# Kernel tuning notes

Measured on AMD Instinct MI355X. Metric: run time of the kernel, lower is better.

## Reference

```python
import jax, jax.numpy as jnp
import numpy as np

B, S, D, H, A = 4, 2048, 512, 8, 64


def setup_inputs() -> dict:
    key = jax.random.key(0)
    ks = jax.random.split(key, 12)
    inv_d = 1.0 / np.sqrt(D)
    inv_ha = 1.0 / np.sqrt(H * A)
    return {
        "query": jax.random.normal(ks[0], (B, S, D), jnp.float32),
        "key": jax.random.normal(ks[1], (B, S, D), jnp.float32),
        "value": jax.random.normal(ks[2], (B, S, D), jnp.float32),
        # stacked per-head projection weights, layout [H, in, out] so y = x @ W + b
        "Wq": jax.random.uniform(ks[3], (H, D, A), jnp.float32, -inv_d, inv_d),
        "bq": jax.random.uniform(ks[4], (H, A), jnp.float32, -inv_d, inv_d),
        "Wk": jax.random.uniform(ks[5], (H, D, A), jnp.float32, -inv_d, inv_d),
        "bk": jax.random.uniform(ks[6], (H, A), jnp.float32, -inv_d, inv_d),
        "Wv": jax.random.uniform(ks[7], (H, D, A), jnp.float32, -inv_d, inv_d),
        "bv": jax.random.uniform(ks[8], (H, A), jnp.float32, -inv_d, inv_d),
        "Wo": jax.random.uniform(ks[9], (H * A, D), jnp.float32, -inv_ha, inv_ha),
        "bo": jax.random.uniform(ks[10], (D,), jnp.float32, -inv_ha, inv_ha),
    }


def reference(query, key, value, Wq, bq, Wk, bk, Wv, bv, Wo, bo):
    b, s, _ = query.shape
    h, _, a = Wq.shape
    # per-head projections, batched across heads: [B,H,S,A]
    q = jnp.einsum("bsd,hda->bhsa", query, Wq) + bq[None, :, None, :]
    k = jnp.einsum("bsd,hda->bhsa", key, Wk) + bk[None, :, None, :]
    v = jnp.einsum("bsd,hda->bhsa", value, Wv) + bv[None, :, None, :]
    scale = a ** 0.5
    scores = jnp.einsum("bhqa,bhka->bhqk", q, k) / scale  # [B,H,S,S]
    # Faithful to original: subsequent_mask has 0.0 on lower tri, -inf above;
    # masked_fill(mask == 0, -1e9) therefore masks the LOWER triangle (incl diag).
    tril = jnp.tril(jnp.ones((s, s), dtype=bool))
    scores = jnp.where(tril, jnp.float32(-1e9), scores)
    attn = jax.nn.softmax(scores, axis=-1)
    out = jnp.einsum("bhqk,bhka->bhqa", attn, v)  # [B,H,S,A]
    # concat heads in order (head-major in feature dim, matching torch.cat dim=-1)
    out = out.transpose(0, 2, 1, 3).reshape(b, s, h * a)
    return out @ Wo + bo
```

## Files before the change

kernel.cpp:

```cpp
#include <hip/hip_runtime.h>
#include <hip/hip_bf16.h>

#define B_ 4
#define S_ 2048
#define D_ 512
#define H_ 8
#define A_ 64

typedef __attribute__((ext_vector_type(8))) __bf16 bf16x8;
typedef __attribute__((ext_vector_type(4))) __bf16 bf16x4;
typedef __attribute__((ext_vector_type(4))) float f32x4;

static __device__ __forceinline__ f32x4 mfma16(bf16x8 a, bf16x8 b, f32x4 c) {
  return __builtin_amdgcn_mfma_f32_16x16x32_bf16(a, b, c, 0, 0, 0);
}

static __device__ __forceinline__ f32x4 zero4() {
  f32x4 z = {0.f, 0.f, 0.f, 0.f};
  return z;
}

#define QSCALE 0.18033688011f

#if __has_builtin(__builtin_amdgcn_exp2f)
#define EXP2(x) __builtin_amdgcn_exp2f(x)
#else
#define EXP2(x) exp2f(x)
#endif

#define GLDS(g, l)                                                      \
  __builtin_amdgcn_global_load_lds(                                     \
      (const __attribute__((address_space(1))) void*)(g),               \
      (__attribute__((address_space(3))) void*)(l), 16, 0, 0)

__global__ void prep_all_kernel(const float* __restrict__ q, const float* __restrict__ k,
                                const float* __restrict__ v,
                                const float* __restrict__ Wq, const float* __restrict__ Wk,
                                const float* __restrict__ Wv, const float* __restrict__ Wo,
                                __bf16* __restrict__ xq, __bf16* __restrict__ xk,
                                __bf16* __restrict__ xv,
                                __bf16* __restrict__ tq, __bf16* __restrict__ tk,
                                __bf16* __restrict__ tv, __bf16* __restrict__ to_) {
  __shared__ float tile[64][65];
  if (blockIdx.x < 12288) {
    int idx = blockIdx.x * 256 + threadIdx.x;
    int which = idx >> 20;
    int i = idx & ((1 << 20) - 1);
    const float4* s = (const float4*)(which == 0 ? q : (which == 1 ? k : v));
    __bf16* d = (which == 0) ? xq : (which == 1 ? xk : xv);
    float4 f = s[i];
    bf16x4 o;
    o.x = (__bf16)f.x; o.y = (__bf16)f.y; o.z = (__bf16)f.z; o.w = (__bf16)f.w;
    *(bf16x4*)(d + 4 * i) = o;
  } else {
    int t = blockIdx.x - 12288;
    if (t < 192) {
      int mat = t >> 6;
      int h = (t >> 3) & 7;
      int d0 = (t & 7) * 64;
      const float* W = (mat == 0) ? Wq : (mat == 1 ? Wk : Wv);
      __bf16* dst = (mat == 0) ? tq : (mat == 1 ? tk : tv);
      float sc = (mat == 0) ? QSCALE : 1.0f;
      int a = threadIdx.x & 63, r0 = threadIdx.x >> 6;
#pragma unroll
      for (int i = 0; i < 16; i++) {
        int dd = r0 * 16 + i;
        tile[dd][a] = W[(h * D_ + d0 + dd) * A_ + a] * sc;
      }
      __syncthreads();
      int dd = threadIdx.x & 63, a0 = threadIdx.x >> 6;
#pragma unroll
      for (int i = 0; i < 16; i++) {
        int a2 = a0 * 16 + i;
        dst[(h * 64 + a2) * D_ + d0 + dd] = (__bf16)tile[dd][a2];
      }
    } else {
      int t2 = t - 192;
      int f0 = (t2 >> 3) * 64, d0 = (t2 & 7) * 64;
      int d = threadIdx.x & 63, r0 = threadIdx.x >> 6;
#pragma unroll
      for (int i = 0; i < 16; i++) {
        int ff = r0 * 16 + i;
        tile[ff][d] = Wo[(f0 + ff) * D_ + d0 + d];
      }
      __syncthreads();
      int f = threadIdx.x & 63, a0 = threadIdx.x >> 6;
#pragma unroll
      for (int i = 0; i < 16; i++) {
        int dd = a0 * 16 + i;
        to_[(d0 + dd) * D_ + f0 + f] = (__bf16)tile[f][dd];
      }
    }
  }
}

__global__ __launch_bounds__(256) void proj_gemm_kernel(
    const __bf16* __restrict__ Xq, const __bf16* __restrict__ Xk, const __bf16* __restrict__ Xv,
    const __bf16* __restrict__ Wtq, const __bf16* __restrict__ Wtk, const __bf16* __restrict__ Wtv,
    const float* __restrict__ bq, const float* __restrict__ bk, const float* __restrict__ bv,
    __bf16* __restrict__ Qb, __bf16* __restrict__ Kb, __bf16* __restrict__ Vtb) {
  int z = blockIdx.z;
  const __bf16* X  = (z == 0) ? Xq  : (z == 1 ? Xk  : Xv);
  const __bf16* Wt = (z == 0) ? Wtq : (z == 1 ? Wtk : Wtv);
  const float* bias = (z == 0) ? bq : (z == 1 ? bk : bv);
  float bscale = (z == 0) ? QSCALE : 1.0f;

  int lane = threadIdx.x & 63, wv = threadIdx.x >> 6;
  int wr = wv >> 1, wc = wv & 1;
  int quad = lane >> 4, lc = lane & 15;
  int M0 = blockIdx.x * 128, N0 = blockIdx.y * 128;
  int m0 = M0 + wr * 64, n0 = N0 + wc * 64;

  __shared__ __align__(16) __bf16 smem[2 * 2 * 128 * 64];
#define AB(buf) (smem + (buf) * 16384)
#define BB(buf) (smem + (buf) * 16384 + 8192)

  int srow = lane >> 3;
  int sg = ((lane & 7) ^ srow) * 8;

#pragma unroll
  for (int i = 0; i < 4; ++i) {
    int r0 = wv * 32 + i * 8;
    GLDS(X  + (M0 + r0 + srow) * D_ + sg, AB(0) + r0 * 64);
    GLDS(Wt + (N0 + r0 + srow) * D_ + sg, BB(0) + r0 * 64);
  }

  f32x4 acc[4][4];
#pragma unroll
  for (int mt = 0; mt < 4; mt++)
#pragma unroll
    for (int nt = 0; nt < 4; nt++) acc[mt][nt] = zero4();

  __syncthreads();

  for (int j = 0; j < 8; ++j) {
    int cb = j & 1;
    if (j < 7) {
      int k0 = (j + 1) * 64;
#pragma unroll
      for (int i = 0; i < 4; ++i) {
        int r0 = wv * 32 + i * 8;
        GLDS(X  + (M0 + r0 + srow) * D_ + k0 + sg, AB(cb ^ 1) + r0 * 64);
        GLDS(Wt + (N0 + r0 + srow) * D_ + k0 + sg, BB(cb ^ 1) + r0 * 64);
      }
    }
    const __bf16* Al = AB(cb);
    const __bf16* Bl = BB(cb);
#pragma unroll
    for (int kk = 0; kk < 2; ++kk) {
      int gp = ((kk * 4 + quad) ^ (lc & 7)) * 8;
      bf16x8 a[4], bb[4];
#pragma unroll
      for (int mt = 0; mt < 4; mt++)
        a[mt] = *(const bf16x8*)(Al + (wr * 64 + mt * 16 + lc) * 64 + gp);
#pragma unroll
      for (int nt = 0; nt < 4; nt++)
        bb[nt] = *(const bf16x8*)(Bl + (wc * 64 + nt * 16 + lc) * 64 + gp);
#pragma unroll
      for (int mt = 0; mt < 4; mt++)
#pragma unroll
        for (int nt = 0; nt < 4; nt++)
          acc[mt][nt] = mfma16(a[mt], bb[nt], acc[mt][nt]);
    }
    __syncthreads();
  }

  __bf16* vlds = smem + wv * (64 * 72);

  int h = n0 >> 6;
  int b = m0 >> 11, s0 = m0 & (S_ - 1);
  if (z < 2) {
#pragma unroll
    for (int nt = 0; nt < 4; nt++) {
      int col = n0 + nt * 16 + lc;
      float bval = bias[col] * bscale;
#pragma unroll
      for (int mt = 0; mt < 4; mt++)
#pragma unroll
        for (int r = 0; r < 4; r++)
          vlds[(mt * 16 + quad * 4 + r) * 72 + nt * 16 + lc] = (__bf16)(acc[mt][nt][r] + bval);
    }
    __asm__ volatile("s_waitcnt lgkmcnt(0)" ::: "memory");
    __bf16* dst = (z == 0) ? Qb : Kb;
#pragma unroll
    for (int it = 0; it < 8; it++) {
      int row = it * 8 + (lane >> 3);
      int c8 = (lane & 7) * 8;
      bf16x8 vv = *(const bf16x8*)(vlds + row * 72 + c8);
      *(bf16x8*)(dst + ((b * H_ + h) * S_ + s0 + row) * A_ + c8) = vv;
    }
  } else {
#pragma unroll
    for (int nt = 0; nt < 4; nt++) {
      int col = n0 + nt * 16 + lc;
      float bval = bias[col];
#pragma unroll
      for (int mt = 0; mt < 4; mt++) {
        bf16x4 pk;
#pragma unroll
        for (int r = 0; r < 4; r++) pk[r] = (__bf16)(acc[mt][nt][r] + bval);
        *(bf16x4*)(vlds + (nt * 16 + lc) * 72 + mt * 16 + quad * 4) = pk;
      }
    }
    __asm__ volatile("s_waitcnt lgkmcnt(0)" ::: "memory");
#pragma unroll
    for (int it = 0; it < 8; it++) {
      int a_l = it * 8 + (lane >> 3);
      int s_l = (lane & 7) * 8;
      bf16x8 vvv = *(const bf16x8*)(vlds + a_l * 72 + s_l);
      *(bf16x8*)(Vtb + ((b * H_ + h) * A_ + a_l) * S_ + s0 + s_l) = vvv;
    }
  }
}

__global__ __launch_bounds__(256, 4) void flash_kernel(const __bf16* __restrict__ Q,
                                                       const __bf16* __restrict__ K,
                                                       const __bf16* __restrict__ Vt,
                                                       __bf16* __restrict__ O) {
  int id = blockIdx.x;
  int xcd = id & 7, slot = id >> 3;
  int bh = xcd * 4 + (slot & 3);
  int beta = slot >> 2;
  int lane = threadIdx.x & 63, wv = threadIdx.x >> 6;
  int quad = lane >> 4, lc = lane & 15;
  int R0 = beta * 128 + wv * 32;
  int ntile = 32 - 2 * beta;
  int t0 = 2 * beta;

  const __bf16* Qp = Q + bh * S_ * A_;
  const __bf16* Kp = K + bh * S_ * A_;
  const __bf16* Vp = Vt + bh * A_ * S_;

  __shared__ __align__(16) __bf16 kvbuf[2][2][64][64];
  __shared__ __align__(16) __bf16 plds_all[4][32][72];
  __bf16* plds = &plds_all[wv][0][0];

  int srow = lane >> 3;
  int sg = ((lane & 7) ^ srow) * 8;

  {
    int kt = t0 << 6;
#pragma unroll
    for (int i = 0; i < 2; ++i) {
      int r0 = wv * 16 + i * 8;
      GLDS(Kp + (kt + r0 + srow) * A_ + sg, &kvbuf[0][0][r0][0]);
      GLDS(Vp + (r0 + srow) * S_ + kt + sg, &kvbuf[0][1][r0][0]);
    }
  }

  bf16x8 qf[2][2];
#pragma unroll
  for (int qt = 0; qt < 2; qt++) {
    qf[qt][0] = *(const bf16x8*)(Qp + (R0 + qt * 16 + lc) * A_ + quad * 8);
    qf[qt][1] = *(const bf16x8*)(Qp + (R0 + qt * 16 + lc) * A_ + 32 + quad * 8);
  }

  f32x4 o[2][4];
  float lsum[2][4];
#pragma unroll
  for (int qt = 0; qt < 2; qt++)
#pragma unroll
    for (int t = 0; t < 4; t++) { o[qt][t] = zero4(); lsum[qt][t] = 0.f; }

  int g0 = (quad ^ (lc & 7)) * 8;
  int g1 = ((quad + 4) ^ (lc & 7)) * 8;

  __syncthreads();

  for (int j = 0; j < ntile; ++j) {
    int t = t0 + j;
    int cb = j & 1;
    if (j + 1 < ntile) {
      int ktn = (t + 1) << 6;
#pragma unroll
      for (int i = 0; i < 2; ++i) {
        int r0 = wv * 16 + i * 8;
        GLDS(Kp + (ktn + r0 + srow) * A_ + sg, &kvbuf[cb ^ 1][0][r0][0]);
        GLDS(Vp + (r0 + srow) * S_ + ktn + sg, &kvbuf[cb ^ 1][1][r0][0]);
      }
    }
    bool skip = (t * 64 + 63 <= R0);
    if (!skip) {
      const __bf16* Kl = &kvbuf[cb][0][0][0];
      const __bf16* Vl = &kvbuf[cb][1][0][0];
      f32x4 sc[2][4];
#pragma unroll
      for (int nt = 0; nt < 4; nt++) {
        int rr = nt * 16 + lc;
        bf16x8 kf0 = *(const bf16x8*)(Kl + rr * 64 + g0);
        bf16x8 kf1 = *(const bf16x8*)(Kl + rr * 64 + g1);
#pragma unroll
        for (int qt = 0; qt < 2; qt++) {
          f32x4 ss = zero4();
          ss = mfma16(qf[qt][0], kf0, ss);
          ss = mfma16(qf[qt][1], kf1, ss);
          sc[qt][nt] = ss;
        }
      }
      if (t * 64 < R0 + 32) {
#pragma unroll
        for (int qt = 0; qt < 2; qt++)
#pragma unroll
          for (int nt = 0; nt < 4; nt++) {
            int col = t * 64 + nt * 16 + lc;
#pragma unroll
            for (int r = 0; r < 4; r++) {
              int row = R0 + qt * 16 + quad * 4 + r;
              float pv = (col <= row) ? 0.0f : EXP2(sc[qt][nt][r]);
              lsum[qt][r] += pv;
              plds[(qt * 16 + quad * 4 + r) * 72 + nt * 16 + lc] = (__bf16)pv;
            }
          }
      } else {
#pragma unroll
        for (int qt = 0; qt < 2; qt++)
#pragma unroll
          for (int nt = 0; nt < 4; nt++)
#pragma unroll
            for (int r = 0; r < 4; r++) {
              float pv = EXP2(sc[qt][nt][r]);
              lsum[qt][r] += pv;
              plds[(qt * 16 + quad * 4 + r) * 72 + nt * 16 + lc] = (__bf16)pv;
            }
      }
      __asm__ volatile("s_waitcnt lgkmcnt(0)" ::: "memory");
      bf16x8 pf[2][2];
#pragma unroll
      for (int qt = 0; qt < 2; qt++) {
        pf[qt][0] = *(const bf16x8*)(plds + (qt * 16 + lc) * 72 + quad * 8);
        pf[qt][1] = *(const bf16x8*)(plds + (qt * 16 + lc) * 72 + 32 + quad * 8);
      }
      __builtin_amdgcn_s_setprio(1);
#pragma unroll
      for (int ot = 0; ot < 4; ot++) {
        int rr = ot * 16 + lc;
        bf16x8 vf0 = *(const bf16x8*)(Vl + rr * 64 + g0);
        bf16x8 vf1 = *(const bf16x8*)(Vl + rr * 64 + g1);
#pragma unroll
        for (int qt = 0; qt < 2; qt++) {
          o[qt][ot] = mfma16(pf[qt][0], vf0, o[qt][ot]);
          o[qt][ot] = mfma16(pf[qt][1], vf1, o[qt][ot]);
        }
      }
      __builtin_amdgcn_s_setprio(0);
    }
    __syncthreads();
  }

#pragma unroll
  for (int qt = 0; qt < 2; qt++)
#pragma unroll
    for (int r = 0; r < 4; r++) {
      float l = lsum[qt][r];
#pragma unroll
      for (int off = 1; off < 16; off <<= 1) l += __shfl_xor(l, off, 64);
      lsum[qt][r] = l;
    }

#pragma unroll
  for (int qt = 0; qt < 2; qt++)
#pragma unroll
    for (int r = 0; r < 4; r++) {
      float rl = 1.0f / lsum[qt][r];
#pragma unroll
      for (int ot = 0; ot < 4; ot++)
        plds[(qt * 16 + quad * 4 + r) * 72 + ot * 16 + lc] = (__bf16)(o[qt][ot][r] * rl);
    }
  __asm__ volatile("s_waitcnt lgkmcnt(0)" ::: "memory");
  int b = bh >> 3, h = bh & 7;
#pragma unroll
  for (int it = 0; it < 4; it++) {
    int row = it * 8 + (lane >> 3);
    int c8 = (lane & 7) * 8;
    int grow = R0 + row;
    if (grow != S_ - 1)
      *(bf16x8*)(O + (b * S_ + grow) * (H_ * A_) + h * 64 + c8) =
          *(const bf16x8*)(plds + row * 72 + c8);
  }
}

__global__ void rowfix_kernel(const __bf16* __restrict__ Vt, __bf16* __restrict__ O) {
  int bh = blockIdx.x;
  int a = blockIdx.y * 8 + (threadIdx.x >> 5);
  int li = threadIdx.x & 31;
  const __bf16* src = Vt + (bh * A_ + a) * S_;
  float s = 0.f;
#pragma unroll
  for (int j = 0; j < 8; j++) {
    bf16x8 vv = *(const bf16x8*)(src + j * 256 + li * 8);
#pragma unroll
    for (int e = 0; e < 8; e++) s += (float)vv[e];
  }
#pragma unroll
  for (int off = 1; off < 32; off <<= 1) s += __shfl_xor(s, off, 64);
  if (li == 0) {
    int b = bh >> 3, h = bh & 7;
    O[(b * S_ + (S_ - 1)) * (H_ * A_) + h * 64 + a] = (__bf16)(s * (1.0f / 2048.0f));
  }
}

__global__ __launch_bounds__(256) void out_gemm_kernel(const __bf16* __restrict__ Ob,
                                                       const __bf16* __restrict__ Wot,
                                                       const float* __restrict__ bo,
                                                       float* __restrict__ out) {
  int lane = threadIdx.x & 63, wv = threadIdx.x >> 6;
  int wr = wv >> 1, wc = wv & 1;
  int quad = lane >> 4, lc = lane & 15;
  int M0 = blockIdx.x * 128, N0 = blockIdx.y * 128;
  int m0 = M0 + wr * 64, n0 = N0 + wc * 64;

  __shared__ __align__(16) __bf16 smem[2 * 2 * 128 * 64];

  int srow = lane >> 3;
  int sg = ((lane & 7) ^ srow) * 8;

#pragma unroll
  for (int i = 0; i < 4; ++i) {
    int r0 = wv * 32 + i * 8;
    GLDS(Ob  + (M0 + r0 + srow) * D_ + sg, AB(0) + r0 * 64);
    GLDS(Wot + (N0 + r0 + srow) * D_ + sg, BB(0) + r0 * 64);
  }

  f32x4 acc[4][4];
#pragma unroll
  for (int mt = 0; mt < 4; mt++)
#pragma unroll
    for (int nt = 0; nt < 4; nt++) acc[mt][nt] = zero4();

  __syncthreads();

  for (int j = 0; j < 8; ++j) {
    int cb = j & 1;
    if (j < 7) {
      int k0 = (j + 1) * 64;
#pragma unroll
      for (int i = 0; i < 4; ++i) {
        int r0 = wv * 32 + i * 8;
        GLDS(Ob  + (M0 + r0 + srow) * D_ + k0 + sg, AB(cb ^ 1) + r0 * 64);
        GLDS(Wot + (N0 + r0 + srow) * D_ + k0 + sg, BB(cb ^ 1) + r0 * 64);
      }
    }
    const __bf16* Al = AB(cb);
    const __bf16* Bl = BB(cb);
#pragma unroll
    for (int kk = 0; kk < 2; ++kk) {
      int gp = ((kk * 4 + quad) ^ (lc & 7)) * 8;
      bf16x8 a[4], bb[4];
#pragma unroll
      for (int mt = 0; mt < 4; mt++)
        a[mt] = *(const bf16x8*)(Al + (wr * 64 + mt * 16 + lc) * 64 + gp);
#pragma unroll
      for (int nt = 0; nt < 4; nt++)
        bb[nt] = *(const bf16x8*)(Bl + (wc * 64 + nt * 16 + lc) * 64 + gp);
#pragma unroll
      for (int mt = 0; mt < 4; mt++)
#pragma unroll
        for (int nt = 0; nt < 4; nt++)
          acc[mt][nt] = mfma16(a[mt], bb[nt], acc[mt][nt]);
    }
    __syncthreads();
  }

#pragma unroll
  for (int nt = 0; nt < 4; nt++) {
    int col = n0 + nt * 16 + lc;
    float bval = bo[col];
#pragma unroll
    for (int mt = 0; mt < 4; mt++)
#pragma unroll
      for (int r = 0; r < 4; r++) {
        int row = m0 + mt * 16 + quad * 4 + r;
        out[row * D_ + col] = acc[mt][nt][r] + bval;
      }
  }
}

extern "C" void kernel_launch(void* const* d_in, const int* in_sizes, int n_in,
                              void* d_out, int out_size, void* d_ws, size_t ws_size,
                              hipStream_t stream) {
  const float* q  = (const float*)d_in[0];
  const float* k  = (const float*)d_in[1];
  const float* v  = (const float*)d_in[2];
  const float* Wq = (const float*)d_in[3];
  const float* bq = (const float*)d_in[4];
  const float* Wk = (const float*)d_in[5];
  const float* bk = (const float*)d_in[6];
  const float* Wv = (const float*)d_in[7];
  const float* bv = (const float*)d_in[8];
  const float* Wo = (const float*)d_in[9];
  const float* bo = (const float*)d_in[10];

  char* ws = (char*)d_ws;
  __bf16* Xq  = (__bf16*)(ws + 0);
  __bf16* Xk  = (__bf16*)(ws + 8388608);
  __bf16* Xv  = (__bf16*)(ws + 16777216);
  __bf16* Wtq = (__bf16*)(ws + 25165824);
  __bf16* Wtk = (__bf16*)(ws + 25690112);
  __bf16* Wtv = (__bf16*)(ws + 26214400);
  __bf16* Wot = (__bf16*)(ws + 26738688);
  __bf16* Qb  = (__bf16*)(ws + 27262976);
  __bf16* Kb  = (__bf16*)(ws + 35651584);
  __bf16* Vtb = (__bf16*)(ws + 44040192);
  __bf16* Ob  = (__bf16*)(ws + 52428800);

  prep_all_kernel<<<12544, 256, 0, stream>>>(q, k, v, Wq, Wk, Wv, Wo,
                                             Xq, Xk, Xv, Wtq, Wtk, Wtv, Wot);
  proj_gemm_kernel<<<dim3(64, 4, 3), 256, 0, stream>>>(Xq, Xk, Xv, Wtq, Wtk, Wtv,
                                                       bq, bk, bv, Qb, Kb, Vtb);
  flash_kernel<<<dim3(512), 256, 0, stream>>>(Qb, Kb, Vtb, Ob);
  rowfix_kernel<<<dim3(32, 8), 256, 0, stream>>>(Vtb, Ob);
  out_gemm_kernel<<<dim3(64, 4), 256, 0, stream>>>(Ob, Wot, bo, (float*)d_out);
}
```

Baseline: 189.9 us.

## Fuse last-row fix into flash kernel and pair heavy/light blocks per CU

Removes the separate rowfix kernel launch and computes the fully-masked last row (the mean of V) inside the flash blocks with beta==15, which have the least attention work. Also remaps block ids so that on each XCD a heavy query tile (small beta) is scheduled alongside a light one (large beta), to even out the causal-triangle load imbalance. This saves a launch and balances work, but the beta==15 blocks now read a full V row-set per head, which lengthens those blocks.

```diff
diff --git a/kernel.cpp b/kernel.cpp
--- a/kernel.cpp
+++ b/kernel.cpp
@@ -219,8 +219,10 @@
                                                        __bf16* __restrict__ O) {
   int id = blockIdx.x;
   int xcd = id & 7, slot = id >> 3;
-  int bh = xcd * 4 + (slot & 3);
-  int beta = slot >> 2;
+  int pair = slot & 31, half = slot >> 5;
+  int pr = pair >> 1;
+  int beta = half ? (15 - pr) : pr;
+  int bh = xcd * 4 + (pair & 1) + 2 * half;
   int lane = threadIdx.x & 63, wv = threadIdx.x >> 6;
   int quad = lane >> 4, lc = lane & 15;
   int R0 = beta * 128 + wv * 32;
@@ -377,25 +379,22 @@
       *(bf16x8*)(O + (b * S_ + grow) * (H_ * A_) + h * 64 + c8) =
           *(const bf16x8*)(plds + row * 72 + c8);
   }
-}
-
-__global__ void rowfix_kernel(const __bf16* __restrict__ Vt, __bf16* __restrict__ O) {
-  int bh = blockIdx.x;
-  int a = blockIdx.y * 8 + (threadIdx.x >> 5);
-  int li = threadIdx.x & 31;
-  const __bf16* src = Vt + (bh * A_ + a) * S_;
-  float s = 0.f;
-#pragma unroll
-  for (int j = 0; j < 8; j++) {
-    bf16x8 vv = *(const bf16x8*)(src + j * 256 + li * 8);
-#pragma unroll
-    for (int e = 0; e < 8; e++) s += (float)vv[e];
-  }
-#pragma unroll
-  for (int off = 1; off < 32; off <<= 1) s += __shfl_xor(s, off, 64);
-  if (li == 0) {
-    int b = bh >> 3, h = bh & 7;
-    O[(b * S_ + (S_ - 1)) * (H_ * A_) + h * 64 + a] = (__bf16)(s * (1.0f / 2048.0f));
+
+  if (beta == 15) {
+    int a = threadIdx.x >> 2;
+    int li = threadIdx.x & 3;
+    const __bf16* src = Vp + a * S_;
+    float ssum = 0.f;
+#pragma unroll 8
+    for (int j2 = 0; j2 < 64; j2++) {
+      bf16x8 vv = *(const bf16x8*)(src + (j2 * 4 + li) * 8);
+#pragma unroll
+      for (int e = 0; e < 8; e++) ssum += (float)vv[e];
+    }
+    ssum += __shfl_xor(ssum, 1, 64);
+    ssum += __shfl_xor(ssum, 2, 64);
+    if (li == 0)
+      O[(b * S_ + (S_ - 1)) * (H_ * A_) + h * 64 + a] = (__bf16)(ssum * (1.0f / 2048.0f));
   }
 }
 
@@ -508,6 +507,5 @@
   proj_gemm_kernel<<<dim3(64, 4, 3), 256, 0, stream>>>(Xq, Xk, Xv, Wtq, Wtk, Wtv,
                                                        bq, bk, bv, Qb, Kb, Vtb);
   flash_kernel<<<dim3(512), 256, 0, stream>>>(Qb, Kb, Vtb, Ob);
-  rowfix_kernel<<<dim3(32, 8), 256, 0, stream>>>(Vtb, Ob);
   out_gemm_kernel<<<dim3(64, 4), 256, 0, stream>>>(Ob, Wot, bo, (float*)d_out);
 }
```

New measurement: 182.9 us. -3.7%, faster.
